# Kernel tuning notes

Measured on AMD Instinct MI355X. Metric: run time of the kernel, lower is better.

## Reference

```python
import jax, jax.numpy as jnp
import numpy as np

C_S, C_Z, C_OUT = 384, 128, 1


def setup_inputs() -> dict:
    key = jax.random.key(0)
    k_s, k_z, k_w = jax.random.split(key, 3)
    b, n = 1, 512
    s = jax.random.normal(k_s, (b, n, C_S), dtype=jnp.float32)
    z = jax.random.normal(k_z, (b, n, n, C_Z), dtype=jnp.float32)
    # Linear(2*c_s + c_z -> c_out); 'final' init is zeros in OpenFold, use
    # small random weights so gradients are non-trivial.
    W = jax.random.normal(k_w, (2 * C_S + C_Z, C_OUT), dtype=jnp.float32) * 0.02
    bias = jnp.zeros((C_OUT,), dtype=jnp.float32)
    return {"s": s, "z": z, "W": W, "b": bias, "start_ligand_ind": 384}


def reference(s, z, W, b, start_ligand_ind):
    # Decompose the linear over the concat [s_i, s_j, z] into three
    # projections; mathematically identical to cat+Linear but avoids
    # materializing the (b, n, n, 2*c_s + c_z) intermediate.
    W_i = W[:C_S]            # (c_s, c_out)
    W_j = W[C_S:2 * C_S]     # (c_s, c_out)
    W_z = W[2 * C_S:]        # (c_z, c_out)
    a_i = jnp.einsum('bnc,co->bno', s, W_i)          # (b, n, c_out)
    a_j = jnp.einsum('bnc,co->bno', s, W_j)          # (b, n, c_out)
    a_z = jnp.einsum('bnmc,co->bnmo', z, W_z)        # (b, n, n, c_out)
    logits = a_i[:, :, None, :] + a_j[:, None, :, :] + a_z + b
    logits = logits + jnp.swapaxes(logits, 1, 2)     # symmetrize over (i, j)
    return logits[:, :start_ligand_ind, start_ligand_ind:]
```

## Files before the change

kernel.cpp:

```cpp
#include <hip/hip_runtime.h>


#define C_S   384
#define C_Z   128
#define N_TOK 512
#define SL    384

__global__ __launch_bounds__(256)
void icn_as_kernel(const float* __restrict__ s,
                   const float* __restrict__ W,
                   const float* __restrict__ bias,
                   float* __restrict__ a_s) {
    const int wave = (int)((blockIdx.x * blockDim.x + threadIdx.x) >> 6);
    const int lane = (int)(threadIdx.x & 63);
    if (wave >= N_TOK) return;
    const float* srow = s + (size_t)wave * C_S;
    float sum = 0.f;
    #pragma unroll
    for (int c0 = 0; c0 < C_S; c0 += 64) {
        const int c = c0 + lane;
        sum += srow[c] * (W[c] + W[C_S + c]);
    }
    #pragma unroll
    for (int off = 32; off; off >>= 1) sum += __shfl_down(sum, off, 64);
    if (lane == 0) a_s[wave] = sum + bias[0];
}

__global__ __launch_bounds__(256)
void icn_main_kernel(const float* __restrict__ z,
                     const float* __restrict__ W,
                     const float* __restrict__ a_s,
                     float* __restrict__ out) {
    const int tid  = (int)(blockIdx.x * blockDim.x + threadIdx.x);
    const int wid  = tid >> 6;
    const int lane = (int)(threadIdx.x & 63);
    const int g0   = wid << 2;
    const int n    = g0 >> 7;
    const int j0   = g0 & 127;
    const int m0   = SL + j0;

    const int  l  = lane & 31;
    const bool lo = lane < 32;

    const float4 wz = ((const float4*)(W + 2 * C_S))[l];

    const float4* za = (const float4*)(z + ((size_t)n * N_TOK + m0) * C_Z);
    const float4 a0 = za[lane];
    const float4 a1 = za[lane + 64];

    const size_t zb_n = (size_t)n * C_Z;
    const float4* b0p = (const float4*)(z + ((size_t)(lo ? m0 : m0 + 1) * N_TOK) * C_Z + zb_n);
    const float4* b1p = (const float4*)(z + ((size_t)(lo ? m0 + 2 : m0 + 3) * N_TOK) * C_Z + zb_n);
    const float4 b0 = b0p[l];
    const float4 b1 = b1p[l];

    float r0 = (a0.x + b0.x) * wz.x + (a0.y + b0.y) * wz.y
             + (a0.z + b0.z) * wz.z + (a0.w + b0.w) * wz.w;
    float r1 = (a1.x + b1.x) * wz.x + (a1.y + b1.y) * wz.y
             + (a1.z + b1.z) * wz.z + (a1.w + b1.w) * wz.w;

    #pragma unroll
    for (int off = 16; off; off >>= 1) {
        r0 += __shfl_xor(r0, off, 64);
        r1 += __shfl_xor(r1, off, 64);
    }

    const float j1 = __shfl(r0, 32, 64);
    const float j3 = __shfl(r1, 32, 64);
    if (lane == 0) {
        const float an = a_s[n];
        const float4 am = *(const float4*)(a_s + m0);
        float4 o;
        o.x = r0 + an + am.x;
        o.y = j1 + an + am.y;
        o.z = r1 + an + am.z;
        o.w = j3 + an + am.w;
        *(float4*)(out + g0) = o;
    }
}

extern "C" void kernel_launch(void* const* d_in, const int* in_sizes, int n_in,
                              void* d_out, int out_size, void* d_ws, size_t ws_size,
                              hipStream_t stream) {
    const float* s    = (const float*)d_in[0];
    const float* z    = (const float*)d_in[1];
    const float* W    = (const float*)d_in[2];
    const float* bias = (const float*)d_in[3];

    float* a_s = (float*)d_ws;

    icn_as_kernel<<<dim3((N_TOK * 64) / 256), 256, 0, stream>>>(s, W, bias, a_s);

    icn_main_kernel<<<dim3(3072), 256, 0, stream>>>(z, W, a_s, (float*)d_out);
}
```

Before: 18.43 us.

## Split main kernel into direct and transposed passes with block-remapped transposed reads

Splits the fused kernel into two launches. Pass A reads the direct z[n, m] rows and writes partial outputs. Pass B reads the transposed z[m, n] rows with a 2D grid, so the four waves in a block touch adjacent n, and it accumulates into the output with a read-modify-write. The aim is better locality for the strided transposed access. The cost is an extra kernel launch and an extra round trip through the output buffer.

```diff
diff --git a/kernel.cpp b/kernel.cpp
--- a/kernel.cpp
+++ b/kernel.cpp
@@ -27,46 +27,34 @@
 }
 
 __global__ __launch_bounds__(256)
-void icn_main_kernel(const float* __restrict__ z,
-                     const float* __restrict__ W,
-                     const float* __restrict__ a_s,
-                     float* __restrict__ out) {
+void icn_passA(const float* __restrict__ z,
+               const float* __restrict__ W,
+               const float* __restrict__ a_s,
+               float* __restrict__ out) {
     const int tid  = (int)(blockIdx.x * blockDim.x + threadIdx.x);
     const int wid  = tid >> 6;
     const int lane = (int)(threadIdx.x & 63);
-    const int g0   = wid << 2;
-    const int n    = g0 >> 7;
-    const int j0   = g0 & 127;
+    const int n    = wid >> 5;
+    const int j0   = (wid & 31) << 2;
     const int m0   = SL + j0;
-
-    const int  l  = lane & 31;
-    const bool lo = lane < 32;
+    const int l    = lane & 31;
 
     const float4 wz = ((const float4*)(W + 2 * C_S))[l];
-
     const float4* za = (const float4*)(z + ((size_t)n * N_TOK + m0) * C_Z);
     const float4 a0 = za[lane];
     const float4 a1 = za[lane + 64];
 
-    const size_t zb_n = (size_t)n * C_Z;
-    const float4* b0p = (const float4*)(z + ((size_t)(lo ? m0 : m0 + 1) * N_TOK) * C_Z + zb_n);
-    const float4* b1p = (const float4*)(z + ((size_t)(lo ? m0 + 2 : m0 + 3) * N_TOK) * C_Z + zb_n);
-    const float4 b0 = b0p[l];
-    const float4 b1 = b1p[l];
-
-    float r0 = (a0.x + b0.x) * wz.x + (a0.y + b0.y) * wz.y
-             + (a0.z + b0.z) * wz.z + (a0.w + b0.w) * wz.w;
-    float r1 = (a1.x + b1.x) * wz.x + (a1.y + b1.y) * wz.y
-             + (a1.z + b1.z) * wz.z + (a1.w + b1.w) * wz.w;
+    float r0 = a0.x * wz.x + a0.y * wz.y + a0.z * wz.z + a0.w * wz.w;
+    float r1 = a1.x * wz.x + a1.y * wz.y + a1.z * wz.z + a1.w * wz.w;
 
     #pragma unroll
     for (int off = 16; off; off >>= 1) {
         r0 += __shfl_xor(r0, off, 64);
         r1 += __shfl_xor(r1, off, 64);
     }
-
     const float j1 = __shfl(r0, 32, 64);
     const float j3 = __shfl(r1, 32, 64);
+
     if (lane == 0) {
         const float an = a_s[n];
         const float4 am = *(const float4*)(a_s + m0);
@@ -75,7 +63,45 @@
         o.y = j1 + an + am.y;
         o.z = r1 + an + am.z;
         o.w = j3 + an + am.w;
-        *(float4*)(out + g0) = o;
+        *(float4*)(out + (n << 7) + j0) = o;
+    }
+}
+
+__global__ __launch_bounds__(256)
+void icn_passB(const float* __restrict__ z,
+               const float* __restrict__ W,
+               float* __restrict__ out) {
+    const int wv   = (int)(threadIdx.x >> 6);
+    const int lane = (int)(threadIdx.x & 63);
+    const int n    = (int)(blockIdx.x << 2) + wv;
+    const int j0   = (int)(blockIdx.y << 2);
+    const int m0   = SL + j0;
+    const int l    = lane & 31;
+    const bool lo  = lane < 32;
+
+    const float4 wz = ((const float4*)(W + 2 * C_S))[l];
+    const size_t zb_n = (size_t)n * C_Z;
+    const float4* b0p = (const float4*)(z + ((size_t)(lo ? m0 : m0 + 1) * N_TOK) * C_Z + zb_n);
+    const float4* b1p = (const float4*)(z + ((size_t)(lo ? m0 + 2 : m0 + 3) * N_TOK) * C_Z + zb_n);
+    const float4 b0 = b0p[l];
+    const float4 b1 = b1p[l];
+
+    float r0 = b0.x * wz.x + b0.y * wz.y + b0.z * wz.z + b0.w * wz.w;
+    float r1 = b1.x * wz.x + b1.y * wz.y + b1.z * wz.z + b1.w * wz.w;
+
+    #pragma unroll
+    for (int off = 16; off; off >>= 1) {
+        r0 += __shfl_xor(r0, off, 64);
+        r1 += __shfl_xor(r1, off, 64);
+    }
+    const float j1 = __shfl(r0, 32, 64);
+    const float j3 = __shfl(r1, 32, 64);
+
+    if (lane == 0) {
+        float4* o = (float4*)(out + (n << 7) + j0);
+        float4 v = *o;
+        v.x += r0; v.y += j1; v.z += r1; v.w += j3;
+        *o = v;
     }
 }
 
@@ -91,5 +117,7 @@
 
     icn_as_kernel<<<dim3((N_TOK * 64) / 256), 256, 0, stream>>>(s, W, bias, a_s);
 
-    icn_main_kernel<<<dim3(3072), 256, 0, stream>>>(z, W, a_s, (float*)d_out);
+    icn_passA<<<dim3(3072), 256, 0, stream>>>(z, W, a_s, (float*)d_out);
+
+    icn_passB<<<dim3(96, 32), 256, 0, stream>>>(z, W, (float*)d_out);
 }
```

Measured after the change: 20.97 us. 13.8% more time.
